# Performance work log

Hardware: AMD Instinct MI355X
Metric: run time of the kernel (lower is better)

The kernel has to match this reference:

```python
import jax, jax.numpy as jnp
import numpy as np

B, D, S = 16, 64, 2048


def setup_inputs() -> dict:
    key = jax.random.key(0)
    kq, kk, kv, km = jax.random.split(key, 4)
    q = jax.random.normal(kq, (B, D, S), dtype=jnp.float32)
    k = jax.random.normal(kk, (B, D, S), dtype=jnp.float32)
    v = jax.random.normal(kv, (B, D, S), dtype=jnp.float32)
    # boolean mask over the [B, Sq, Sk] score matrix (True -> filled with -1000)
    mask = jax.random.bernoulli(km, 0.1, (B, S, S))
    return {"q": q, "k": k, "v": v, "mask": mask}


def reference(q, k, v, mask):
    dim = jnp.asarray(D, dtype=q.dtype)
    # scores[b, s, t] = sum_d q[b, d, s] * k[b, d, t] / sqrt(D)
    scores = jnp.einsum("bds,bdt->bst", q, k) / jnp.sqrt(dim)
    scores = jnp.where(mask, jnp.asarray(-1000.0, dtype=scores.dtype), scores)
    # NOTE: softmax over dim=1 (the QUERY axis), faithful to nn.Softmax(dim=1)
    attn = jax.nn.softmax(scores, axis=1)
    # out[b, s, d] = sum_t attn[b, s, t] * v[b, d, t]
    out = jnp.einsum("bst,bdt->bsd", attn, v)
    return out
```

## Files before the change

kernel.cpp:

```cpp
#include <hip/hip_runtime.h>
#include <hip/hip_bf16.h>
#include <stdint.h>


namespace {
constexpr int B = 16;
constexpr int D = 64;
constexpr int S = 2048;
constexpr float SCALE = 0.125f;

typedef __attribute__((ext_vector_type(8))) short short8;
typedef __attribute__((ext_vector_type(4))) float f32x4;

constexpr size_t WS_FLAG  = 0;
constexpr size_t WS_LINV  = 256;
constexpr size_t WS_LPART = 256 + 131072;
constexpr size_t WS_QT    = 655616;
constexpr size_t WS_KT    = 4849920;
constexpr size_t WS_VB    = 9044224;
constexpr size_t WS_MPACK = 13238528;
constexpr size_t WS_OPART = 21627136;
constexpr size_t NEED_OLD = 13238528;
constexpr size_t NEED_T1  = 21627136;
constexpr size_t NEED_T2  = 38404352;
}

__device__ __forceinline__ bool mask_at(const void* mask, int mode, size_t idx) {
    if (mode == 1) return ((const int*)mask)[idx] != 0;
    if (mode == 2) return ((const float*)mask)[idx] != 0.0f;
    return ((const unsigned char*)mask)[idx] != 0;
}

__device__ __forceinline__ uint16_t f2bf(float f) {
    unsigned int u = __float_as_uint(f);
    unsigned int r = (u + 0x7fffu + ((u >> 16) & 1u)) >> 16;
    return (uint16_t)r;
}
__device__ __forceinline__ unsigned int pack2(float a, float b) {
    return (unsigned int)f2bf(a) | ((unsigned int)f2bf(b) << 16);
}

__device__ __forceinline__ int swz(int row, int colByte) {
    return row * 128 + (colByte ^ ((row & 7) << 4));
}

__device__ __forceinline__ void gll16(const void* g, void* l) {
    __builtin_amdgcn_global_load_lds(
        (const __attribute__((address_space(1))) void*)g,
        (__attribute__((address_space(3))) void*)l, 16, 0, 0);
}

__device__ __forceinline__ void stage_tile(const char* srcRows, size_t rowStrideB,
                                           unsigned char* dst, int tid) {
    const int lane = tid & 63, w = tid >> 6;
    const int lrow = lane >> 3;
    const int slot = (lane & 7) ^ lrow;
    #pragma unroll
    for (int c = 0; c < 2; ++c) {
        const int row = 16 * w + 8 * c + lrow;
        gll16(srcRows + (size_t)row * rowStrideB + slot * 16,
              dst + (16 * w + 8 * c) * 128);
    }
}

__device__ __forceinline__ f32x4 mfma16(short8 a, short8 b, f32x4 c) {
    return __builtin_amdgcn_mfma_f32_16x16x32_bf16(a, b, c, 0, 0, 0);
}

__global__ void probe_mask_kernel(const unsigned char* __restrict__ mask,
                                  int* __restrict__ flag)
{
    __shared__ int c0s, c123s;
    if (threadIdx.x == 0) { c0s = 0; c123s = 0; }
    __syncthreads();
    int c0 = 0, c123 = 0;
    for (int f = threadIdx.x; f < 65536; f += 256) {
        const int nz = (mask[f] != 0) ? 1 : 0;
        if ((f & 3) == 0) c0 += nz; else c123 += nz;
    }
    atomicAdd(&c0s, c0);
    atomicAdd(&c123s, c123);
    __syncthreads();
    if (threadIdx.x == 0) {
        int mode = 0;
        if (c123s == 0) mode = 1;
        else if (c0s == 0) mode = 2;
        *flag = mode;
    }
}

__global__ __launch_bounds__(256, 2)
void transpose_cvt_kernel(const float* __restrict__ q, const float* __restrict__ k,
                          uint16_t* __restrict__ qT, uint16_t* __restrict__ kT)
{
    __shared__ float ts[64][65];
    const int tid = threadIdx.x;
    const int s0 = blockIdx.x * 64;
    const int b  = blockIdx.y;
    const float* src = blockIdx.z ? k : q;
    uint16_t*    dst = blockIdx.z ? kT : qT;

    {
        const int d = tid >> 2, c = tid & 3;
        const float* row = src + ((size_t)b * D + d) * S + s0 + c * 16;
        #pragma unroll
        for (int i = 0; i < 4; ++i) {
            float4 v4 = *(const float4*)(row + 4 * i);
            ts[c * 16 + 4 * i + 0][d] = v4.x;
            ts[c * 16 + 4 * i + 1][d] = v4.y;
            ts[c * 16 + 4 * i + 2][d] = v4.z;
            ts[c * 16 + 4 * i + 3][d] = v4.w;
        }
    }
    __syncthreads();
    {
        const int srow = tid >> 2, p = tid & 3;
        uint16_t tmp[16];
        #pragma unroll
        for (int j = 0; j < 16; ++j) tmp[j] = f2bf(ts[srow][p * 16 + j]);
        uint16_t* drow = dst + ((size_t)b * S + s0 + srow) * 64 + p * 16;
        *(uint4*)drow       = ((const uint4*)tmp)[0];
        *((uint4*)drow + 1) = ((const uint4*)tmp)[1];
    }
}

__global__ void cvt_v_kernel(const float* __restrict__ v, uint16_t* __restrict__ vb)
{
    const size_t i = ((size_t)blockIdx.x * 256 + threadIdx.x) * 4;
    float4 v4 = *(const float4*)(v + i);
    uint16_t t4[4] = {f2bf(v4.x), f2bf(v4.y), f2bf(v4.z), f2bf(v4.w)};
    *(uint2*)(vb + i) = *(const uint2*)t4;
}

__global__ __launch_bounds__(256, 4)
void pass1_kernel(const uint16_t* __restrict__ qT, const uint16_t* __restrict__ kT,
                  const void* __restrict__ mask, const int* __restrict__ flagp,
                  float* __restrict__ lpart, unsigned long long* __restrict__ mpackT)
{
    __shared__ __align__(16) unsigned char ksb[64 * 128];
    __shared__ __align__(16) unsigned char qsb[64 * 128];
    __shared__ unsigned short mbits[64][4];
    __shared__ float red[4][64];

    const int tid = threadIdx.x;
    const int lane = tid & 63, w = tid >> 6;
    const int l = lane & 15, hh = lane >> 4;
    const int t0 = blockIdx.x * 64;
    const int chunk = blockIdx.y;
    const int b = blockIdx.z;
    const int mode = *flagp;

    const int row_m = tid >> 2, cq = tid & 3;
    const size_t mrow_base = ((size_t)b * S + row_m) * S + t0 + cq * 16;

    stage_tile((const char*)(kT + ((size_t)b * S + t0) * 64), 128, ksb, tid);

    int4  mr4[4];
    uint4 mr1;
    auto load_mtile = [&](int sbase) {
        if (mode != 0) {
            const int4* p = (const int4*)((const int*)mask + mrow_base + (size_t)sbase * S);
            mr4[0] = p[0]; mr4[1] = p[1]; mr4[2] = p[2]; mr4[3] = p[3];
        } else {
            mr1 = *(const uint4*)((const unsigned char*)mask + mrow_base + (size_t)sbase * S);
        }
    };
    auto pack_mtile = [&]() -> unsigned int {
        unsigned int bits = 0;
        if (mode != 0) {
            #pragma unroll
            for (int i = 0; i < 4; ++i) {
                bits |= (mr4[i].x ? 1u : 0u) << (4 * i + 0);
                bits |= (mr4[i].y ? 1u : 0u) << (4 * i + 1);
                bits |= (mr4[i].z ? 1u : 0u) << (4 * i + 2);
                bits |= (mr4[i].w ? 1u : 0u) << (4 * i + 3);
            }
        } else {
            const unsigned int u[4] = {mr1.x, mr1.y, mr1.z, mr1.w};
            #pragma unroll
            for (int c = 0; c < 4; ++c) {
                bits |= ((u[c] & 0x000000FFu) ? 1u : 0u) << (4 * c + 0);
                bits |= ((u[c] & 0x0000FF00u) ? 1u : 0u) << (4 * c + 1);
                bits |= ((u[c] & 0x00FF0000u) ? 1u : 0u) << (4 * c + 2);
                bits |= ((u[c] & 0xFF000000u) ? 1u : 0u) << (4 * c + 3);
            }
        }
        return bits;
    };

    load_mtile(chunk * 512);
    __syncthreads();

    float colacc[4] = {0.f, 0.f, 0.f, 0.f};

    for (int it = 0; it < 8; ++it) {
        const int sbase = chunk * 512 + it * 64;
        __syncthreads();
        stage_tile((const char*)(qT + ((size_t)b * S + sbase) * 64), 128, qsb, tid);

        const unsigned int bits = pack_mtile();
        if (it < 7) load_mtile(sbase + 64);
        mbits[row_m][cq] = (unsigned short)bits;
        __syncthreads();

        if (tid < 64) {
            const unsigned long long word =
                (unsigned long long)mbits[tid][0]
                | ((unsigned long long)mbits[tid][1] << 16)
                | ((unsigned long long)mbits[tid][2] << 32)
                | ((unsigned long long)mbits[tid][3] << 48);
            mpackT[((size_t)b * 32 + (t0 >> 6)) * S + sbase + tid] = word;
        }

        short8 A0 = *(const short8*)&qsb[swz(16 * w + l, 0  + hh * 16)];
        short8 A1 = *(const short8*)&qsb[swz(16 * w + l, 64 + hh * 16)];
        const int srow_l = 16 * w + 4 * hh;

        #pragma unroll
        for (int tf = 0; tf < 4; ++tf) {
            const short8 B0 = *(const short8*)&ksb[swz(tf * 16 + l, 0  + hh * 16)];
            const short8 B1 = *(const short8*)&ksb[swz(tf * 16 + l, 64 + hh * 16)];
            f32x4 c4 = {0.f, 0.f, 0.f, 0.f};
            c4 = mfma16(A0, B0, c4);
            c4 = mfma16(A1, B1, c4);
            #pragma unroll
            for (int r = 0; r < 4; ++r) {
                if (!((mbits[srow_l + r][tf] >> l) & 1))
                    colacc[tf] += __expf(c4[r] * SCALE);
            }
        }
    }

    #pragma unroll
    for (int tf = 0; tf < 4; ++tf) {
        colacc[tf] += __shfl_xor(colacc[tf], 16);
        colacc[tf] += __shfl_xor(colacc[tf], 32);
    }
    if (lane < 16) {
        #pragma unroll
        for (int tf = 0; tf < 4; ++tf) red[w][tf * 16 + lane] = colacc[tf];
    }
    __syncthreads();
    if (tid < 64) {
        const float s = red[0][tid] + red[1][tid] + red[2][tid] + red[3][tid];
        lpart[(size_t)chunk * (B * S) + (size_t)b * S + t0 + tid] = s;
    }
}

__global__ void linv_kernel(const float* __restrict__ lpart, float* __restrict__ linv)
{
    const int i = blockIdx.x * 256 + threadIdx.x;
    const float s = lpart[i] + lpart[B * S + i] + lpart[2 * B * S + i] + lpart[3 * B * S + i];
    linv[i] = 1.0f / s;
}

__global__ __launch_bounds__(256, 2)
void pass2_kernel(const uint16_t* __restrict__ qT, const uint16_t* __restrict__ kT,
                  const uint16_t* __restrict__ vb,
                  const unsigned long long* __restrict__ mpackT,
                  const float* __restrict__ linv, float* __restrict__ dst, int tspan)
{
    __shared__ __align__(16) unsigned char qsb[64 * 128];
    __shared__ __align__(16) unsigned char ksb[64 * 128];
    __shared__ __align__(16) unsigned char vsb[64 * 128];
    __shared__ __align__(16) unsigned char ptb[64 * 128];
    __shared__ unsigned long long mrow2[64];
    __shared__ float linv_s[64];

    const int tid = threadIdx.x;
    const int lane = tid & 63, w = tid >> 6;
    const int l = lane & 15, hh = lane >> 4;
    const int s0 = blockIdx.x * 64;
    const int tc = blockIdx.y;
    const int b = blockIdx.z;
    const int t_begin = tc * tspan, t_end = t_begin + tspan;
    float* outp = dst + (size_t)tc * (B * S * D);

    stage_tile((const char*)(qT + ((size_t)b * S + s0) * 64), 128, qsb, tid);
    __syncthreads();

    short8 QB[4][2];
    #pragma unroll
    for (int sf = 0; sf < 4; ++sf)
        #pragma unroll
        for (int kh = 0; kh < 2; ++kh)
            QB[sf][kh] = *(const short8*)&qsb[swz(sf * 16 + l, kh * 64 + hh * 16)];

    f32x4 oacc[4];
    #pragma unroll
    for (int df = 0; df < 4; ++df) oacc[df] = (f32x4){0.f, 0.f, 0.f, 0.f};

    for (int t0 = t_begin; t0 < t_end; t0 += 64) {
        stage_tile((const char*)(kT + ((size_t)b * S + t0) * 64), 128, ksb, tid);
        stage_tile((const char*)(vb + (size_t)b * D * S + t0), (size_t)S * 2, vsb, tid);
        if (tid < 64) {
            mrow2[tid]  = mpackT[((size_t)b * 32 + (t0 >> 6)) * S + s0 + tid];
            linv_s[tid] = linv[(size_t)b * S + t0 + tid];
        }
        __syncthreads();

        short8 KA0 = *(const short8*)&ksb[swz(16 * w + l, 0  + hh * 16)];
        short8 KA1 = *(const short8*)&ksb[swz(16 * w + l, 64 + hh * 16)];
        float lv[4];
        #pragma unroll
        for (int r = 0; r < 4; ++r) lv[r] = linv_s[16 * w + 4 * hh + r];

        #pragma unroll
        for (int sf = 0; sf < 4; ++sf) {
            f32x4 c4 = {0.f, 0.f, 0.f, 0.f};
            c4 = mfma16(KA0, QB[sf][0], c4);
            c4 = mfma16(KA1, QB[sf][1], c4);
            const unsigned long long bits = mrow2[sf * 16 + l];
            float pv[4];
            #pragma unroll
            for (int r = 0; r < 4; ++r) {
                const int tloc = 16 * w + 4 * hh + r;
                pv[r] = ((bits >> tloc) & 1ull) ? 0.f : __expf(c4[r] * SCALE) * lv[r];
            }
            const int row = sf * 16 + l;
            const int cb = (32 * w + 8 * hh);
            *(uint2*)&ptb[row * 128 + (cb ^ ((row & 7) << 4))] =
                make_uint2(pack2(pv[0], pv[1]), pack2(pv[2], pv[3]));
        }
        __syncthreads();

        short8 PA0 = *(const short8*)&ptb[swz(16 * w + l, 0  + hh * 16)];
        short8 PA1 = *(const short8*)&ptb[swz(16 * w + l, 64 + hh * 16)];
        #pragma unroll
        for (int df = 0; df < 4; ++df) {
            short8 VB0 = *(const short8*)&vsb[swz(df * 16 + l, 0  + hh * 16)];
            short8 VB1 = *(const short8*)&vsb[swz(df * 16 + l, 64 + hh * 16)];
            oacc[df] = mfma16(PA0, VB0, oacc[df]);
            oacc[df] = mfma16(PA1, VB1, oacc[df]);
        }
        __syncthreads();
    }

    #pragma unroll
    for (int df = 0; df < 4; ++df)
        #pragma unroll
        for (int r = 0; r < 4; ++r)
            outp[((size_t)b * S + s0 + 16 * w + 4 * hh + r) * D + df * 16 + l] = oacc[df][r];
}

__global__ void opart_reduce_kernel(const float* __restrict__ p, float* __restrict__ out)
{
    const size_t i = ((size_t)blockIdx.x * 256 + threadIdx.x) * 4;
    float4 a = *(const float4*)(p + i);
    float4 b = *(const float4*)(p + (size_t)B * S * D + i);
    *(float4*)(out + i) = make_float4(a.x + b.x, a.y + b.y, a.z + b.z, a.w + b.w);
}

__global__ __launch_bounds__(256, 2)
void pass1_old_kernel(const uint16_t* __restrict__ qT, const uint16_t* __restrict__ kT,
                      const void* __restrict__ mask, const int* __restrict__ flagp,
                      float* __restrict__ lpart)
{
    __shared__ __align__(16) unsigned char ksb[64 * 128];
    __shared__ __align__(16) unsigned char qsb[64 * 128];
    __shared__ float red[4][64];
    const int tid = threadIdx.x;
    const int lane = tid & 63, w = tid >> 6;
    const int l = lane & 15, hh = lane >> 4;
    const int t0 = blockIdx.x * 64;
    const int chunk = blockIdx.y;
    const int b = blockIdx.z;
    const int mode = *flagp;
    const size_t mbase = (size_t)b * S * S;

    stage_tile((const char*)(kT + ((size_t)b * S + t0) * 64), 128, ksb, tid);
    __syncthreads();
    short8 BF[4][2];
    #pragma unroll
    for (int tf = 0; tf < 4; ++tf)
        #pragma unroll
        for (int kh = 0; kh < 2; ++kh)
            BF[tf][kh] = *(const short8*)&ksb[swz(tf * 16 + l, kh * 64 + hh * 16)];
    float colacc[4] = {0.f, 0.f, 0.f, 0.f};
    for (int it = 0; it < 8; ++it) {
        const int sbase = chunk * 512 + it * 64;
        __syncthreads();
        stage_tile((const char*)(qT + ((size_t)b * S + sbase) * 64), 128, qsb, tid);
        __syncthreads();
        short8 A0 = *(const short8*)&qsb[swz(16 * w + l, 0  + hh * 16)];
        short8 A1 = *(const short8*)&qsb[swz(16 * w + l, 64 + hh * 16)];
        #pragma unroll
        for (int tf = 0; tf < 4; ++tf) {
            f32x4 c4 = {0.f, 0.f, 0.f, 0.f};
            c4 = mfma16(A0, BF[tf][0], c4);
            c4 = mfma16(A1, BF[tf][1], c4);
            const int t = t0 + tf * 16 + l;
            const int srow = sbase + 16 * w + 4 * hh;
            #pragma unroll
            for (int r = 0; r < 4; ++r)
                if (!mask_at(mask, mode, mbase + (size_t)(srow + r) * S + t))
                    colacc[tf] += __expf(c4[r] * SCALE);
        }
    }
    #pragma unroll
    for (int tf = 0; tf < 4; ++tf) {
        colacc[tf] += __shfl_xor(colacc[tf], 16);
        colacc[tf] += __shfl_xor(colacc[tf], 32);
    }
    if (lane < 16) {
        #pragma unroll
        for (int tf = 0; tf < 4; ++tf) red[w][tf * 16 + lane] = colacc[tf];
    }
    __syncthreads();
    if (tid < 64) {
        const float s = red[0][tid] + red[1][tid] + red[2][tid] + red[3][tid];
        lpart[(size_t)chunk * (B * S) + (size_t)b * S + t0 + tid] = s;
    }
}

__global__ __launch_bounds__(256, 2)
void pass2_old_kernel(const uint16_t* __restrict__ qT, const uint16_t* __restrict__ kT,
                      const uint16_t* __restrict__ vb, const void* __restrict__ mask,
                      const int* __restrict__ flagp, const float* __restrict__ linv,
                      float* __restrict__ out)
{
    __shared__ __align__(16) unsigned char qsb[64 * 128];
    __shared__ __align__(16) unsigned char ksb[64 * 128];
    __shared__ __align__(16) unsigned char vsb[64 * 128];
    __shared__ __align__(16) unsigned char ptb[64 * 128];
    __shared__ unsigned short mbits[64][4];
    __shared__ float linv_s[64];
    const int tid = threadIdx.x;
    const int lane = tid & 63, w = tid >> 6;
    const int l = lane & 15, hh = lane >> 4;
    const int s0 = blockIdx.x * 64;
    const int b = blockIdx.y;
    const int mode = *flagp;
    const size_t mbase = (size_t)b * S * S;

    stage_tile((const char*)(qT + ((size_t)b * S + s0) * 64), 128, qsb, tid);
    __syncthreads();
    short8 QB[4][2];
    #pragma unroll
    for (int sf = 0; sf < 4; ++sf)
        #pragma unroll
        for (int kh = 0; kh < 2; ++kh)
            QB[sf][kh] = *(const short8*)&qsb[swz(sf * 16 + l, kh * 64 + hh * 16)];
    f32x4 oacc[4];
    #pragma unroll
    for (int df = 0; df < 4; ++df) oacc[df] = (f32x4){0.f, 0.f, 0.f, 0.f};

    for (int t0 = 0; t0 < S; t0 += 64) {
        stage_tile((const char*)(kT + ((size_t)b * S + t0) * 64), 128, ksb, tid);
        stage_tile((const char*)(vb + (size_t)b * D * S + t0), (size_t)S * 2, vsb, tid);
        {
            const int srow = tid >> 2, c = tid & 3;
            const size_t base = mbase + (size_t)(s0 + srow) * S + t0 + c * 16;
            unsigned int bits = 0;
            #pragma unroll
            for (int j = 0; j < 16; ++j)
                bits |= (mask_at(mask, mode, base + j) ? 1u : 0u) << j;
            mbits[srow][c] = (unsigned short)bits;
        }
        if (tid < 64) linv_s[tid] = linv[(size_t)b * S + t0 + tid];
        __syncthreads();

        short8 KA0 = *(const short8*)&ksb[swz(16 * w + l, 0  + hh * 16)];
        short8 KA1 = *(const short8*)&ksb[swz(16 * w + l, 64 + hh * 16)];
        float lv[4];
        #pragma unroll
        for (int r = 0; r < 4; ++r) lv[r] = linv_s[16 * w + 4 * hh + r];
        #pragma unroll
        for (int sf = 0; sf < 4; ++sf) {
            f32x4 c4 = {0.f, 0.f, 0.f, 0.f};
            c4 = mfma16(KA0, QB[sf][0], c4);
            c4 = mfma16(KA1, QB[sf][1], c4);
            const unsigned int mb = (unsigned int)mbits[sf * 16 + l][w] >> (4 * hh);
            float pv[4];
            #pragma unroll
            for (int r = 0; r < 4; ++r)
                pv[r] = ((mb >> r) & 1u) ? 0.f : __expf(c4[r] * SCALE) * lv[r];
            const int row = sf * 16 + l;
            const int cb = (32 * w + 8 * hh);
            *(uint2*)&ptb[row * 128 + (cb ^ ((row & 7) << 4))] =
                make_uint2(pack2(pv[0], pv[1]), pack2(pv[2], pv[3]));
        }
        __syncthreads();
        short8 PA0 = *(const short8*)&ptb[swz(16 * w + l, 0  + hh * 16)];
        short8 PA1 = *(const short8*)&ptb[swz(16 * w + l, 64 + hh * 16)];
        #pragma unroll
        for (int df = 0; df < 4; ++df) {
            short8 VB0 = *(const short8*)&vsb[swz(df * 16 + l, 0  + hh * 16)];
            short8 VB1 = *(const short8*)&vsb[swz(df * 16 + l, 64 + hh * 16)];
            oacc[df] = mfma16(PA0, VB0, oacc[df]);
            oacc[df] = mfma16(PA1, VB1, oacc[df]);
        }
        __syncthreads();
    }
    #pragma unroll
    for (int df = 0; df < 4; ++df)
        #pragma unroll
        for (int r = 0; r < 4; ++r)
            out[((size_t)b * S + s0 + 16 * w + 4 * hh + r) * D + df * 16 + l] = oacc[df][r];
}

__global__ __launch_bounds__(256, 2)
void colsum_fb(const float* __restrict__ q, const float* __restrict__ k,
               const void* __restrict__ mask, const int* __restrict__ flagp,
               float* __restrict__ lsums)
{
    __shared__ __align__(16) float qs[128][68];
    __shared__ __align__(16) float ks[64][68];
    __shared__ float lred[32][66];
    const int tid = threadIdx.x;
    const int b = blockIdx.y;
    const int t0 = blockIdx.x * 64;
    const int mode = *flagp;
    {
        const int tl = tid & 63, d0 = tid >> 6;
        #pragma unroll
        for (int i = 0; i < 16; ++i) { const int d = d0 + i * 4; ks[tl][d] = k[(b * D + d) * S + t0 + tl]; }
    }
    const int tq = tid & 7, sq = tid >> 3;
    float lacc[8];
    #pragma unroll
    for (int j = 0; j < 8; ++j) lacc[j] = 0.f;
    const size_t mbase = (size_t)b * S * S;
    for (int s0 = 0; s0 < S; s0 += 128) {
        __syncthreads();
        {
            const int sl = tid & 127, d0 = tid >> 7;
            #pragma unroll
            for (int i = 0; i < 32; ++i) { const int d = d0 + i * 2; qs[sl][d] = q[(b * D + d) * S + s0 + sl]; }
        }
        __syncthreads();
        float acc[4][8];
        #pragma unroll
        for (int jj = 0; jj < 4; ++jj)
            #pragma unroll
            for (int j = 0; j < 8; ++j) acc[jj][j] = 0.f;
        #pragma unroll
        for (int dblk = 0; dblk < 16; ++dblk) {
            float4 q4[4];
            #pragma unroll
            for (int jj = 0; jj < 4; ++jj) q4[jj] = *(const float4*)&qs[sq + 32 * jj][dblk * 4];
            #pragma unroll
            for (int j = 0; j < 8; ++j) {
                const float4 k4 = *(const float4*)&ks[tq + 8 * j][dblk * 4];
                #pragma unroll
                for (int jj = 0; jj < 4; ++jj)
                    acc[jj][j] += q4[jj].x * k4.x + q4[jj].y * k4.y + q4[jj].z * k4.z + q4[jj].w * k4.w;
            }
        }
        #pragma unroll
        for (int jj = 0; jj < 4; ++jj) {
            const int sg = s0 + sq + 32 * jj;
            const size_t ridx = mbase + (size_t)sg * S + t0;
            #pragma unroll
            for (int j = 0; j < 8; ++j)
                if (!mask_at(mask, mode, ridx + tq + 8 * j)) lacc[j] += __expf(acc[jj][j] * SCALE);
        }
    }
    __syncthreads();
    #pragma unroll
    for (int j = 0; j < 8; ++j) lred[sq][tq + 8 * j] = lacc[j];
    __syncthreads();
    if (tid < 64) {
        float s = 0.f;
        #pragma unroll
        for (int i = 0; i < 32; ++i) s += lred[i][tid];
        lsums[b * S + t0 + tid] = s;
    }
}

__global__ __launch_bounds__(256, 2)
void attn_out_fb(const float* __restrict__ q, const float* __restrict__ k,
                 const float* __restrict__ v, const void* __restrict__ mask,
                 const int* __restrict__ flagp, const float* __restrict__ lsums,
                 float* __restrict__ out)
{
    __shared__ __align__(16) float qs[64][68];
    __shared__ __align__(16) float kw[64][68];
    __shared__ __align__(16) float pt[64][68];
    __shared__ float linv_sh[64];
    const int tid = threadIdx.x;
    const int b = blockIdx.y;
    const int s0 = blockIdx.x * 64;
    const int mode = *flagp;
    {
        const int sl = tid & 63, d0 = tid >> 6;
        #pragma unroll
        for (int i = 0; i < 16; ++i) { const int d = d0 + i * 4; qs[sl][d] = q[(b * D + d) * S + s0 + sl]; }
    }
    const int tq = tid & 7, sq = tid >> 3;
    float oacc[2][8];
    #pragma unroll
    for (int jj = 0; jj < 2; ++jj)
        #pragma unroll
        for (int dd = 0; dd < 8; ++dd) oacc[jj][dd] = 0.f;
    const size_t mbase = (size_t)b * S * S;
    for (int t0 = 0; t0 < S; t0 += 64) {
        __syncthreads();
        if (tid < 64) linv_sh[tid] = 1.f / lsums[b * S + t0 + tid];
        {
            const int tl = tid & 63, d0 = tid >> 6;
            #pragma unroll
            for (int i = 0; i < 16; ++i) { const int d = d0 + i * 4; kw[tl][d] = k[(b * D + d) * S + t0 + tl]; }
        }
        __syncthreads();
        float sc[2][8];
        #pragma unroll
        for (int jj = 0; jj < 2; ++jj)
            #pragma unroll
            for (int j = 0; j < 8; ++j) sc[jj][j] = 0.f;
        #pragma unroll
        for (int dblk = 0; dblk < 16; ++dblk) {
            float4 q4[2];
            #pragma unroll
            for (int jj = 0; jj < 2; ++jj) q4[jj] = *(const float4*)&qs[sq + 32 * jj][dblk * 4];
            #pragma unroll
            for (int j = 0; j < 8; ++j) {
                const float4 k4 = *(const float4*)&kw[tq + 8 * j][dblk * 4];
                #pragma unroll
                for (int jj = 0; jj < 2; ++jj)
                    sc[jj][j] += q4[jj].x * k4.x + q4[jj].y * k4.y + q4[jj].z * k4.z + q4[jj].w * k4.w;
            }
        }
        #pragma unroll
        for (int jj = 0; jj < 2; ++jj) {
            const int sg = s0 + sq + 32 * jj;
            const size_t ridx = mbase + (size_t)sg * S + t0;
            #pragma unroll
            for (int j = 0; j < 8; ++j) {
                const int tl = tq + 8 * j;
                const bool msk = mask_at(mask, mode, ridx + tl);
                pt[tl][sq + 32 * jj] = msk ? 0.f : __expf(sc[jj][j] * SCALE) * linv_sh[tl];
            }
        }
        __syncthreads();
        {
            const int tl = tid & 63, d0 = tid >> 6;
            #pragma unroll
            for (int i = 0; i < 16; ++i) { const int d = d0 + i * 4; kw[tl][d] = v[(b * D + d) * S + t0 + tl]; }
        }
        __syncthreads();
        #pragma unroll 8
        for (int t = 0; t < 64; ++t) {
            const float2 p2 = *(const float2*)&pt[t][sq * 2];
            const float4 w0 = *(const float4*)&kw[t][tq * 8];
            const float4 w1 = *(const float4*)&kw[t][tq * 8 + 4];
            oacc[0][0] += p2.x * w0.x; oacc[0][1] += p2.x * w0.y; oacc[0][2] += p2.x * w0.z; oacc[0][3] += p2.x * w0.w;
            oacc[0][4] += p2.x * w1.x; oacc[0][5] += p2.x * w1.y; oacc[0][6] += p2.x * w1.z; oacc[0][7] += p2.x * w1.w;
            oacc[1][0] += p2.y * w0.x; oacc[1][1] += p2.y * w0.y; oacc[1][2] += p2.y * w0.z; oacc[1][3] += p2.y * w0.w;
            oacc[1][4] += p2.y * w1.x; oacc[1][5] += p2.y * w1.y; oacc[1][6] += p2.y * w1.z; oacc[1][7] += p2.y * w1.w;
        }
    }
    #pragma unroll
    for (int jj = 0; jj < 2; ++jj) {
        float* dst = out + ((size_t)(b * S + s0 + sq * 2 + jj)) * D + tq * 8;
        *(float4*)dst = make_float4(oacc[jj][0], oacc[jj][1], oacc[jj][2], oacc[jj][3]);
        *(float4*)(dst + 4) = make_float4(oacc[jj][4], oacc[jj][5], oacc[jj][6], oacc[jj][7]);
    }
}

extern "C" void kernel_launch(void* const* d_in, const int* in_sizes, int n_in,
                              void* d_out, int out_size, void* d_ws, size_t ws_size,
                              hipStream_t stream) {
    const float* q = (const float*)d_in[0];
    const float* k = (const float*)d_in[1];
    const float* v = (const float*)d_in[2];
    const void*  mask = d_in[3];
    float* out = (float*)d_out;
    char* ws = (char*)d_ws;

    int* flag = (int*)(ws + WS_FLAG);
    probe_mask_kernel<<<1, 256, 0, stream>>>((const unsigned char*)mask, flag);

    if (ws_size >= NEED_T1) {
        float*    linv  = (float*)(ws + WS_LINV);
        float*    lpart = (float*)(ws + WS_LPART);
        uint16_t* qT    = (uint16_t*)(ws + WS_QT);
        uint16_t* kT    = (uint16_t*)(ws + WS_KT);
        uint16_t* vb    = (uint16_t*)(ws + WS_VB);
        unsigned long long* mpackT = (unsigned long long*)(ws + WS_MPACK);

        transpose_cvt_kernel<<<dim3(S / 64, B, 2), 256, 0, stream>>>(q, k, qT, kT);
        cvt_v_kernel<<<(B * D * S) / (256 * 4), 256, 0, stream>>>(v, vb);
        pass1_kernel<<<dim3(S / 64, 4, B), 256, 0, stream>>>(qT, kT, mask, flag, lpart, mpackT);
        linv_kernel<<<(B * S) / 256, 256, 0, stream>>>(lpart, linv);

        if (ws_size >= NEED_T2) {
            float* opart = (float*)(ws + WS_OPART);
            pass2_kernel<<<dim3(S / 64, 2, B), 256, 0, stream>>>(
                qT, kT, vb, mpackT, linv, opart, S / 2);
            opart_reduce_kernel<<<(B * S * D) / (256 * 4), 256, 0, stream>>>(opart, out);
        } else {
            pass2_kernel<<<dim3(S / 64, 1, B), 256, 0, stream>>>(
                qT, kT, vb, mpackT, linv, out, S);
        }
    } else if (ws_size >= NEED_OLD) {
        float*    linv  = (float*)(ws + WS_LINV);
        float*    lpart = (float*)(ws + WS_LPART);
        uint16_t* qT    = (uint16_t*)(ws + WS_QT);
        uint16_t* kT    = (uint16_t*)(ws + WS_KT);
        uint16_t* vb    = (uint16_t*)(ws + WS_VB);
        transpose_cvt_kernel<<<dim3(S / 64, B, 2), 256, 0, stream>>>(q, k, qT, kT);
        cvt_v_kernel<<<(B * D * S) / (256 * 4), 256, 0, stream>>>(v, vb);
        pass1_old_kernel<<<dim3(S / 64, 4, B), 256, 0, stream>>>(qT, kT, mask, flag, lpart);
        linv_kernel<<<(B * S) / 256, 256, 0, stream>>>(lpart, linv);
        pass2_old_kernel<<<dim3(S / 64, B), 256, 0, stream>>>(qT, kT, vb, mask, flag, linv, out);
    } else {
        float* lsums = (float*)(ws + WS_LINV);
        dim3 grid(S / 64, B);
        colsum_fb<<<grid, 256, 0, stream>>>(q, k, mask, flag, lsums);
        attn_out_fb<<<grid, 256, 0, stream>>>(q, k, v, mask, flag, lsums, out);
    }
}
```

Baseline: 172.0 us.

## Double-buffer Q and K/V tiles in pass kernels and fuse V conversion into prep

Pass1 now double-buffers the Q tile and prefetches the next Q tile and mask tile while computing on the current one. Pass2 double-buffers the K, V, mask-row and linv tiles so the next tile's loads overlap the PV MFMA step, which drops one barrier per iteration. The separate V bf16 conversion launch is merged into the transpose kernel as a third grid slice, saving one launch. Extra shared memory in both pass kernels may reduce occupancy.

```diff
diff --git a/kernel.cpp b/kernel.cpp
--- a/kernel.cpp
+++ b/kernel.cpp
@@ -90,16 +90,31 @@
 }
 
 __global__ __launch_bounds__(256, 2)
-void transpose_cvt_kernel(const float* __restrict__ q, const float* __restrict__ k,
-                          uint16_t* __restrict__ qT, uint16_t* __restrict__ kT)
+void prep_kernel(const float* __restrict__ q, const float* __restrict__ k,
+                 const float* __restrict__ v,
+                 uint16_t* __restrict__ qT, uint16_t* __restrict__ kT,
+                 uint16_t* __restrict__ vb)
 {
     __shared__ float ts[64][65];
     const int tid = threadIdx.x;
     const int s0 = blockIdx.x * 64;
     const int b  = blockIdx.y;
+
+    if (blockIdx.z == 2) {
+        const int d = tid >> 2, c = tid & 3;
+        const float* row = v + ((size_t)b * D + d) * S + s0 + c * 16;
+        uint16_t*   orow = vb + ((size_t)b * D + d) * S + s0 + c * 16;
+        #pragma unroll
+        for (int i = 0; i < 4; ++i) {
+            float4 v4 = *(const float4*)(row + 4 * i);
+            uint16_t t4[4] = {f2bf(v4.x), f2bf(v4.y), f2bf(v4.z), f2bf(v4.w)};
+            *(uint2*)(orow + 4 * i) = *(const uint2*)t4;
+        }
+        return;
+    }
+
     const float* src = blockIdx.z ? k : q;
     uint16_t*    dst = blockIdx.z ? kT : qT;
-
     {
         const int d = tid >> 2, c = tid & 3;
         const float* row = src + ((size_t)b * D + d) * S + s0 + c * 16;
@@ -124,21 +139,13 @@
     }
 }
 
-__global__ void cvt_v_kernel(const float* __restrict__ v, uint16_t* __restrict__ vb)
-{
-    const size_t i = ((size_t)blockIdx.x * 256 + threadIdx.x) * 4;
-    float4 v4 = *(const float4*)(v + i);
-    uint16_t t4[4] = {f2bf(v4.x), f2bf(v4.y), f2bf(v4.z), f2bf(v4.w)};
-    *(uint2*)(vb + i) = *(const uint2*)t4;
-}
-
 __global__ __launch_bounds__(256, 4)
 void pass1_kernel(const uint16_t* __restrict__ qT, const uint16_t* __restrict__ kT,
                   const void* __restrict__ mask, const int* __restrict__ flagp,
                   float* __restrict__ lpart, unsigned long long* __restrict__ mpackT)
 {
     __shared__ __align__(16) unsigned char ksb[64 * 128];
-    __shared__ __align__(16) unsigned char qsb[64 * 128];
+    __shared__ __align__(16) unsigned char qsb[2][64 * 128];
     __shared__ unsigned short mbits[64][4];
     __shared__ float red[4][64];
 
@@ -152,8 +159,6 @@
 
     const int row_m = tid >> 2, cq = tid & 3;
     const size_t mrow_base = ((size_t)b * S + row_m) * S + t0 + cq * 16;
-
-    stage_tile((const char*)(kT + ((size_t)b * S + t0) * 64), 128, ksb, tid);
 
     int4  mr4[4];
     uint4 mr1;
@@ -188,19 +193,21 @@
         return bits;
     };
 
+    stage_tile((const char*)(kT + ((size_t)b * S + t0) * 64), 128, ksb, tid);
+    stage_tile((const char*)(qT + ((size_t)b * S + chunk * 512) * 64), 128, qsb[0], tid);
     load_mtile(chunk * 512);
-    __syncthreads();
 
     float colacc[4] = {0.f, 0.f, 0.f, 0.f};
 
     for (int it = 0; it < 8; ++it) {
+        const int cur = it & 1;
         const int sbase = chunk * 512 + it * 64;
-        __syncthreads();
-        stage_tile((const char*)(qT + ((size_t)b * S + sbase) * 64), 128, qsb, tid);
+
+        __syncthreads();
 
         const unsigned int bits = pack_mtile();
-        if (it < 7) load_mtile(sbase + 64);
         mbits[row_m][cq] = (unsigned short)bits;
+
         __syncthreads();
 
         if (tid < 64) {
@@ -212,8 +219,14 @@
             mpackT[((size_t)b * 32 + (t0 >> 6)) * S + sbase + tid] = word;
         }
 
-        short8 A0 = *(const short8*)&qsb[swz(16 * w + l, 0  + hh * 16)];
-        short8 A1 = *(const short8*)&qsb[swz(16 * w + l, 64 + hh * 16)];
+        if (it < 7) {
+            stage_tile((const char*)(qT + ((size_t)b * S + sbase + 64) * 64), 128,
+                       qsb[cur ^ 1], tid);
+            load_mtile(sbase + 64);
+        }
+
+        short8 A0 = *(const short8*)&qsb[cur][swz(16 * w + l, 0  + hh * 16)];
+        short8 A1 = *(const short8*)&qsb[cur][swz(16 * w + l, 64 + hh * 16)];
         const int srow_l = 16 * w + 4 * hh;
 
         #pragma unroll
@@ -236,6 +249,7 @@
         colacc[tf] += __shfl_xor(colacc[tf], 16);
         colacc[tf] += __shfl_xor(colacc[tf], 32);
     }
+    __syncthreads();
     if (lane < 16) {
         #pragma unroll
         for (int tf = 0; tf < 4; ++tf) red[w][tf * 16 + lane] = colacc[tf];
@@ -261,11 +275,11 @@
                   const float* __restrict__ linv, float* __restrict__ dst, int tspan)
 {
     __shared__ __align__(16) unsigned char qsb[64 * 128];
-    __shared__ __align__(16) unsigned char ksb[64 * 128];
-    __shared__ __align__(16) unsigned char vsb[64 * 128];
+    __shared__ __align__(16) unsigned char ksb[2][64 * 128];
+    __shared__ __align__(16) unsigned char vsb[2][64 * 128];
     __shared__ __align__(16) unsigned char ptb[64 * 128];
-    __shared__ unsigned long long mrow2[64];
-    __shared__ float linv_s[64];
+    __shared__ unsigned long long mrow2[2][64];
+    __shared__ float linv_s[2][64];
 
     const int tid = threadIdx.x;
     const int lane = tid & 63, w = tid >> 6;
@@ -273,10 +287,17 @@
     const int s0 = blockIdx.x * 64;
     const int tc = blockIdx.y;
     const int b = blockIdx.z;
-    const int t_begin = tc * tspan, t_end = t_begin + tspan;
+    const int t_begin = tc * tspan;
+    const int niter = tspan / 64;
     float* outp = dst + (size_t)tc * (B * S * D);
 
     stage_tile((const char*)(qT + ((size_t)b * S + s0) * 64), 128, qsb, tid);
+    stage_tile((const char*)(kT + ((size_t)b * S + t_begin) * 64), 128, ksb[0], tid);
+    stage_tile((const char*)(vb + (size_t)b * D * S + t_begin), (size_t)S * 2, vsb[0], tid);
+    if (tid < 64) {
+        mrow2[0][tid]  = mpackT[((size_t)b * 32 + (t_begin >> 6)) * S + s0 + tid];
+        linv_s[0][tid] = linv[(size_t)b * S + t_begin + tid];
+    }
     __syncthreads();
 
     short8 QB[4][2];
@@ -290,27 +311,22 @@
     #pragma unroll
     for (int df = 0; df < 4; ++df) oacc[df] = (f32x4){0.f, 0.f, 0.f, 0.f};
 
-    for (int t0 = t_begin; t0 < t_end; t0 += 64) {
-        stage_tile((const char*)(kT + ((size_t)b * S + t0) * 64), 128, ksb, tid);
-        stage_tile((const char*)(vb + (size_t)b * D * S + t0), (size_t)S * 2, vsb, tid);
-        if (tid < 64) {
-            mrow2[tid]  = mpackT[((size_t)b * 32 + (t0 >> 6)) * S + s0 + tid];
-            linv_s[tid] = linv[(size_t)b * S + t0 + tid];
-        }
-        __syncthreads();
-
-        short8 KA0 = *(const short8*)&ksb[swz(16 * w + l, 0  + hh * 16)];
-        short8 KA1 = *(const short8*)&ksb[swz(16 * w + l, 64 + hh * 16)];
+    for (int i = 0; i < niter; ++i) {
+        const int cur = i & 1, nxt = cur ^ 1;
+        const int t0 = t_begin + i * 64;
+
+        short8 KA0 = *(const short8*)&ksb[cur][swz(16 * w + l, 0  + hh * 16)];
+        short8 KA1 = *(const short8*)&ksb[cur][swz(16 * w + l, 64 + hh * 16)];
         float lv[4];
         #pragma unroll
-        for (int r = 0; r < 4; ++r) lv[r] = linv_s[16 * w + 4 * hh + r];
+        for (int r = 0; r < 4; ++r) lv[r] = linv_s[cur][16 * w + 4 * hh + r];
 
         #pragma unroll
         for (int sf = 0; sf < 4; ++sf) {
             f32x4 c4 = {0.f, 0.f, 0.f, 0.f};
             c4 = mfma16(KA0, QB[sf][0], c4);
             c4 = mfma16(KA1, QB[sf][1], c4);
-            const unsigned long long bits = mrow2[sf * 16 + l];
+            const unsigned long long bits = mrow2[cur][sf * 16 + l];
             float pv[4];
             #pragma unroll
             for (int r = 0; r < 4; ++r) {
@@ -324,12 +340,25 @@
         }
         __syncthreads();
 
+        if (i + 1 < niter) {
+            const int tn = t0 + 64;
+            stage_tile((const char*)(kT + ((size_t)b * S + tn) * 64), 128, ksb[nxt], tid);
+            stage_tile((const char*)(vb + (size_t)b * D * S + tn), (size_t)S * 2, vsb[nxt], tid);
+            if (tid < 64) {
+                const unsigned long long mw =
+                    mpackT[((size_t)b * 32 + (tn >> 6)) * S + s0 + tid];
+                const float lw = linv[(size_t)b * S + tn + tid];
+                mrow2[nxt][tid]  = mw;
+                linv_s[nxt][tid] = lw;
+            }
+        }
+
         short8 PA0 = *(const short8*)&ptb[swz(16 * w + l, 0  + hh * 16)];
         short8 PA1 = *(const short8*)&ptb[swz(16 * w + l, 64 + hh * 16)];
         #pragma unroll
         for (int df = 0; df < 4; ++df) {
-            short8 VB0 = *(const short8*)&vsb[swz(df * 16 + l, 0  + hh * 16)];
-            short8 VB1 = *(const short8*)&vsb[swz(df * 16 + l, 64 + hh * 16)];
+            short8 VB0 = *(const short8*)&vsb[cur][swz(df * 16 + l, 0  + hh * 16)];
+            short8 VB1 = *(const short8*)&vsb[cur][swz(df * 16 + l, 64 + hh * 16)];
             oacc[df] = mfma16(PA0, VB0, oacc[df]);
             oacc[df] = mfma16(PA1, VB1, oacc[df]);
         }
@@ -349,6 +378,48 @@
     float4 a = *(const float4*)(p + i);
     float4 b = *(const float4*)(p + (size_t)B * S * D + i);
     *(float4*)(out + i) = make_float4(a.x + b.x, a.y + b.y, a.z + b.z, a.w + b.w);
+}
+
+__global__ __launch_bounds__(256, 2)
+void transpose_cvt_kernel(const float* __restrict__ q, const float* __restrict__ k,
+                          uint16_t* __restrict__ qT, uint16_t* __restrict__ kT)
+{
+    __shared__ float ts[64][65];
+    const int tid = threadIdx.x;
+    const int s0 = blockIdx.x * 64;
+    const int b  = blockIdx.y;
+    const float* src = blockIdx.z ? k : q;
+    uint16_t*    dst = blockIdx.z ? kT : qT;
+    {
+        const int d = tid >> 2, c = tid & 3;
+        const float* row = src + ((size_t)b * D + d) * S + s0 + c * 16;
+        #pragma unroll
+        for (int i = 0; i < 4; ++i) {
+            float4 v4 = *(const float4*)(row + 4 * i);
+            ts[c * 16 + 4 * i + 0][d] = v4.x;
+            ts[c * 16 + 4 * i + 1][d] = v4.y;
+            ts[c * 16 + 4 * i + 2][d] = v4.z;
+            ts[c * 16 + 4 * i + 3][d] = v4.w;
+        }
+    }
+    __syncthreads();
+    {
+        const int srow = tid >> 2, p = tid & 3;
+        uint16_t tmp[16];
+        #pragma unroll
+        for (int j = 0; j < 16; ++j) tmp[j] = f2bf(ts[srow][p * 16 + j]);
+        uint16_t* drow = dst + ((size_t)b * S + s0 + srow) * 64 + p * 16;
+        *(uint4*)drow       = ((const uint4*)tmp)[0];
+        *((uint4*)drow + 1) = ((const uint4*)tmp)[1];
+    }
+}
+
+__global__ void cvt_v_kernel(const float* __restrict__ v, uint16_t* __restrict__ vb)
+{
+    const size_t i = ((size_t)blockIdx.x * 256 + threadIdx.x) * 4;
+    float4 v4 = *(const float4*)(v + i);
+    uint16_t t4[4] = {f2bf(v4.x), f2bf(v4.y), f2bf(v4.z), f2bf(v4.w)};
+    *(uint2*)(vb + i) = *(const uint2*)t4;
 }
 
 __global__ __launch_bounds__(256, 2)
@@ -679,8 +750,7 @@
         uint16_t* vb    = (uint16_t*)(ws + WS_VB);
         unsigned long long* mpackT = (unsigned long long*)(ws + WS_MPACK);
 
-        transpose_cvt_kernel<<<dim3(S / 64, B, 2), 256, 0, stream>>>(q, k, qT, kT);
-        cvt_v_kernel<<<(B * D * S) / (256 * 4), 256, 0, stream>>>(v, vb);
+        prep_kernel<<<dim3(S / 64, B, 3), 256, 0, stream>>>(q, k, v, qT, kT, vb);
         pass1_kernel<<<dim3(S / 64, 4, B), 256, 0, stream>>>(qT, kT, mask, flag, lpart, mpackT);
         linv_kernel<<<(B * S) / 256, 256, 0, stream>>>(lpart, linv);
 
```

New measurement: 180.2 us. +4.7%, slower.
